# Kernel optimization log

Measured on AMD Instinct MI355X. Metric: run time of the kernel, lower is better.

## Reference

```python
import jax, jax.numpy as jnp
import numpy as np

N = 500_000      # evaluation points
M = 8            # Nmode
K = 4            # Clebsch branches
NPSI = 256       # psi grid points
X0 = 0.0
H = 1.0 / (NPSI - 1)


def _cubic_interp(f, x):
    """Cubic Hermite spline (C1, FD slopes) on a uniform psi grid, extrapolating.
    f: [NPSI, C] table, x: [N] query points -> [N, C]."""
    u = (x - X0) / H
    i = jnp.clip(jnp.floor(u).astype(jnp.int32), 0, NPSI - 2)
    s = (u - i.astype(x.dtype))[:, None]           # local coord, may be outside [0,1] (extrap)
    d = jnp.gradient(f, axis=0) / H                # FD derivatives [NPSI, C]
    f0, f1, d0, d1 = f[i], f[i + 1], d[i], d[i + 1]
    s2 = s * s
    s3 = s2 * s
    return ((2 * s3 - 3 * s2 + 1) * f0 + (s3 - 2 * s2 + s) * H * d0
            + (-2 * s3 + 3 * s2) * f1 + (s3 - s2) * H * d1)


def setup_inputs() -> dict:
    key = jax.random.key(0)
    ks = jax.random.split(key, 12)
    pg = jnp.linspace(0.0, 1.0, NPSI, dtype=jnp.float32)
    inp = {
        "t": jnp.float32(0.5),
        "psi": jax.random.uniform(ks[0], (N,), jnp.float32, 0.05, 0.95),
        "theta": jax.random.uniform(ks[1], (N,), jnp.float32, -jnp.pi, jnp.pi),
        "varphi": jax.random.uniform(ks[2], (N,), jnp.float32, 0.0, 2 * jnp.pi),
        # smooth Clebsch profiles on the psi grid (safety factor q and alpha offset)
        "q_vals": (1.0 + 2.5 * pg ** 2).astype(jnp.float32),
        "aoff_vals": (0.3 * jnp.sin(2 * jnp.pi * pg)).astype(jnp.float32),
        "theta0": jax.random.uniform(ks[3], (M,), jnp.float32, -jnp.pi, jnp.pi),
        "omega": jax.random.uniform(ks[4], (M,), jnp.float32, 0.5, 2.0),
        "psi0": jax.random.uniform(ks[5], (M,), jnp.float32, 0.2, 0.8),
        "psi_scale": jax.random.uniform(ks[6], (M,), jnp.float32, 0.05, 0.15),
        "alpha_scale": jax.random.uniform(ks[7], (M,), jnp.float32, 0.2, 0.6),
        "gh_coefs": 0.5 * jax.random.normal(ks[8], (M, 4, 6), jnp.float32),
        "n": jax.random.randint(ks[9], (M,), 1, 12, jnp.int32),
    }
    return inp


def reference(t, psi, theta, varphi, q_vals, aoff_vals, theta0, omega, psi0,
              psi_scale, alpha_scale, gh_coefs, n):
    # Clebsch mapping: alpha_k(psi, theta) = q(psi) * (theta + 2*pi*k) + alpha_off(psi)
    qa = _cubic_interp(jnp.stack([q_vals, aoff_vals], axis=-1), psi)  # [N,2]
    q, aoff = qa[:, 0], qa[:, 1]
    kk = 2 * jnp.pi * jnp.arange(K, dtype=psi.dtype)
    alpha = q[:, None] * (theta[:, None] + kk[None, :]) + aoff[:, None]    # [N,K]
    # alpha0(psi; mode) table built from the Clebsch profiles (mirrors __init__)
    alpha0_grid = q_vals[:, None] * theta0[None, :] + aoff_vals[:, None]   # [NPSI,M]
    alpha0 = _cubic_interp(alpha0_grid, psi)                               # [N,M]

    x = (psi[:, None] - psi0) / psi_scale                                  # [N,M]
    y = (alpha[:, None, :] - alpha0[:, :, None]) / alpha_scale[None, :, None]  # [N,M,K]
    g = jnp.exp(-0.5 * (x[:, :, None] ** 2 + y ** 2))                      # [N,M,K]

    c = gh_coefs  # [M,4,6]
    h10 = x[:, :, None, None]
    h01 = y[:, :, :, None]
    h20 = (4 * x ** 2 - 2)[:, :, None, None]
    h11 = (x[:, :, None] * y)[:, :, :, None]
    h02 = (4 * y ** 2 - 2)[:, :, :, None]
    p = (c[None, :, None, :, 0] + c[None, :, None, :, 1] * h10
         + c[None, :, None, :, 2] * h01 + c[None, :, None, :, 3] * h20
         + c[None, :, None, :, 4] * h11 + c[None, :, None, :, 5] * h02)    # [N,M,K,4]
    p = p * g[:, :, :, None]

    nf = n.astype(psi.dtype)
    # alpha - alpha0 == y * alpha_scale
    phase = omega[None, :, None] * t - nf[None, :, None] * (
        varphi[:, None, None] - y * alpha_scale[None, :, None])            # [N,M,K]
    cp, sp = jnp.cos(phase), jnp.sin(phase)
    phi = jnp.sum(p[..., 0] * cp - p[..., 1] * sp, axis=(1, 2))            # [N]
    apar = jnp.sum(p[..., 2] * cp - p[..., 3] * sp, axis=(1, 2))           # [N]
    return phi, apar
```

## Files before the change

kernel.cpp:

```cpp
#include <hip/hip_runtime.h>

#define NPSI 256
#define MM 8
#define KK 4

typedef float v2f __attribute__((ext_vector_type(2)));

#if __has_builtin(__builtin_amdgcn_exp2f)
#define EXP2F(x) __builtin_amdgcn_exp2f(x)
#else
#define EXP2F(x) exp2f(x)
#endif
#define SIN_REV(x) __builtin_amdgcn_sinf(x)
#define COS_REV(x) __builtin_amdgcn_cosf(x)

#define VFMA(a,b,c) __builtin_elementwise_fma((v2f)(a),(v2f)(b),(v2f)(c))

__device__ inline float cubic_q(const float* __restrict__ q_vals, float psi) {
    float u = psi * (float)(NPSI - 1);
    int   i = (int)floorf(u);
    i = min(max(i, 0), NPSI - 2);
    float s  = u - (float)i;
    float f0 = q_vals[i];
    float f1 = q_vals[i + 1];
    float d0 = (i == 0)        ? (f1 - f0) : 0.5f * (f1 - q_vals[i - 1]);
    float d1 = (i == NPSI - 2) ? (f1 - f0) : 0.5f * (q_vals[i + 2] - f0);
    float s2 = s * s, s3 = s2 * s;
    return (2.f * s3 - 3.f * s2 + 1.f) * f0
         + (s3 - 2.f * s2 + s)         * d0
         + (-2.f * s3 + 3.f * s2)      * f1
         + (s3 - s2)                   * d1;
}

__global__ __launch_bounds__(256, 8) void eik_kernel(
    const float* __restrict__ t_ptr,
    const float* __restrict__ psi_a,
    const float* __restrict__ theta_a,
    const float* __restrict__ varphi_a,
    const float* __restrict__ q_vals,
    const float* __restrict__ theta0_a,
    const float* __restrict__ omega_a,
    const float* __restrict__ psi0_a,
    const float* __restrict__ psi_scale_a,
    const float* __restrict__ alpha_scale_a,
    const float* __restrict__ gh_a,
    const int*   __restrict__ n_a,
    float* __restrict__ out,
    int N)
{
    const int gid = blockIdx.x * blockDim.x + threadIdx.x;
    if (gid >= N) return;

    const float INV2PI = 0.15915494309189533577f;
    const float TWO_PI = 6.28318530717958647692f;
    const float NEXPC  = -0.72134752044448170368f;

    const float t     = t_ptr[0];
    const float psi   = psi_a[gid];
    const float theta = theta_a[gid];
    const float vp    = varphi_a[gid] * INV2PI;

    const float q    = cubic_q(q_vals, psi);
    const float q2pi = q * TWO_PI;
    const float tt   = t * INV2PI;

    v2f phi = (v2f)0.f, apar = (v2f)0.f;

    #pragma unroll 1
    for (int mp = 0; mp < MM / 2; ++mp) {
        const int m = 2 * mp;
        const v2f theta0 = *(const v2f*)(theta0_a + m);
        const v2f omega  = *(const v2f*)(omega_a + m);
        const v2f psi0   = *(const v2f*)(psi0_a + m);
        const v2f psc    = *(const v2f*)(psi_scale_a + m);
        const v2f asc    = *(const v2f*)(alpha_scale_a + m);
        v2f inv_ps, inv_as, nf;
        inv_ps.x = __builtin_amdgcn_rcpf(psc.x);
        inv_ps.y = __builtin_amdgcn_rcpf(psc.y);
        inv_as.x = __builtin_amdgcn_rcpf(asc.x);
        inv_as.y = __builtin_amdgcn_rcpf(asc.y);
        nf.x = (float)n_a[m];
        nf.y = (float)n_a[m + 1];
        const float* cA = gh_a + m * 24;
        const float* cB = gh_a + (m + 1) * 24;

        const v2f x  = ((v2f)psi - psi0) * inv_ps;
        const v2f x2 = x * x;
        const v2f x4 = 4.f * x2;

        v2f pa[4], pb[4], pf[4];
        #pragma unroll
        for (int comp = 0; comp < 4; ++comp) {
            const v2f c0 = { cA[comp*6+0], cB[comp*6+0] };
            const v2f c1 = { cA[comp*6+1], cB[comp*6+1] };
            const v2f c2 = { cA[comp*6+2], cB[comp*6+2] };
            const v2f c3 = { cA[comp*6+3], cB[comp*6+3] };
            const v2f c4 = { cA[comp*6+4], cB[comp*6+4] };
            const v2f c5 = { cA[comp*6+5], cB[comp*6+5] };
            const v2f a0 = VFMA((v2f)(-2.f), c3 + c5, c0);
            pa[comp] = VFMA(c3, x4, VFMA(c1, x, a0));
            pb[comp] = VFMA(c4, x, c2);
            pf[comp] = c5;
        }

        const v2f dth  = (v2f)theta - theta0;
        const v2f qdth = q * dth;
        v2f y          = qdth * inv_as;
        const v2f dy   = q2pi * inv_as;
        const v2f dphr = nf * q;
        const v2f p0r  = VFMA(nf, qdth * INV2PI,
                              VFMA(omega, (v2f)tt, -nf * vp));

        v2f cp, sp, cd, sd;
        cp.x = COS_REV(p0r.x);  cp.y = COS_REV(p0r.y);
        sp.x = SIN_REV(p0r.x);  sp.y = SIN_REV(p0r.y);
        cd.x = COS_REV(dphr.x); cd.y = COS_REV(dphr.y);
        sd.x = SIN_REV(dphr.x); sd.y = SIN_REV(dphr.y);

        #pragma unroll
        for (int k = 0; k < KK; ++k) {
            const v2f t2 = VFMA(y, y, x2);
            const v2f y4 = VFMA((v2f)4.f, t2, -x4);
            const v2f ta = t2 * NEXPC;
            v2f g;
            g.x = EXP2F(ta.x);
            g.y = EXP2F(ta.y);
            const v2f gc = g * cp;
            const v2f gs = g * sp;
            const v2f p0 = VFMA(pf[0], y4, VFMA(pb[0], y, pa[0]));
            const v2f p1 = VFMA(pf[1], y4, VFMA(pb[1], y, pa[1]));
            const v2f p2 = VFMA(pf[2], y4, VFMA(pb[2], y, pa[2]));
            const v2f p3 = VFMA(pf[3], y4, VFMA(pb[3], y, pa[3]));
            phi  = VFMA(p0, gc, phi);
            phi  = VFMA(-p1, gs, phi);
            apar = VFMA(p2, gc, apar);
            apar = VFMA(-p3, gs, apar);
            if (k < KK - 1) {
                const v2f ncp = VFMA(cp, cd, -(sp * sd));
                const v2f nsp = VFMA(sp, cd,  cp * sd);
                cp = ncp; sp = nsp;
                y = y + dy;
            }
        }
    }

    out[gid]     = phi.x + phi.y;
    out[N + gid] = apar.x + apar.y;
}

extern "C" void kernel_launch(void* const* d_in, const int* in_sizes, int n_in,
                              void* d_out, int out_size, void* d_ws, size_t ws_size,
                              hipStream_t stream) {
    const float* t       = (const float*)d_in[0];
    const float* psi     = (const float*)d_in[1];
    const float* theta   = (const float*)d_in[2];
    const float* varphi  = (const float*)d_in[3];
    const float* q_vals  = (const float*)d_in[4];
    const float* theta0  = (const float*)d_in[6];
    const float* omega   = (const float*)d_in[7];
    const float* psi0    = (const float*)d_in[8];
    const float* psc     = (const float*)d_in[9];
    const float* asc     = (const float*)d_in[10];
    const float* gh      = (const float*)d_in[11];
    const int*   n_arr   = (const int*)d_in[12];

    const int N = in_sizes[1];
    float* out = (float*)d_out;

    const int block = 256;
    const int grid  = (N + block - 1) / block;
    eik_kernel<<<grid, block, 0, stream>>>(t, psi, theta, varphi, q_vals,
                                           theta0, omega, psi0, psc, asc,
                                           gh, n_arr, out, N);
}
```

Before: 97.26 us.

## Precompute per-mode constants in a prep kernel and batch exp evaluations

Adds a tiny prep kernel that writes per-mode constants (reciprocals of the scales, the folded polynomial coefficient, n as float) into a packed, interleaved workspace table. The main kernel then reads them as v2f pairs instead of gathering scalars and recomputing reciprocals and coefficient sums in every thread. The exp2 calls for all K branches are also hoisted into a separate loop ahead of the accumulation, to expose more independent transcendental work. The occupancy hint drops from 8 to 4 waves, which allows more registers per thread. The cost is an extra kernel launch and a workspace dependency.

```diff
diff --git a/kernel.cpp b/kernel.cpp
--- a/kernel.cpp
+++ b/kernel.cpp
@@ -3,6 +3,8 @@
 #define NPSI 256
 #define MM 8
 #define KK 4
+#define NMP (MM / 2)
+#define TBF (NMP * 60)
 
 typedef float v2f __attribute__((ext_vector_type(2)));
 
@@ -32,12 +34,7 @@
          + (s3 - s2)                   * d1;
 }
 
-__global__ __launch_bounds__(256, 8) void eik_kernel(
-    const float* __restrict__ t_ptr,
-    const float* __restrict__ psi_a,
-    const float* __restrict__ theta_a,
-    const float* __restrict__ varphi_a,
-    const float* __restrict__ q_vals,
+__global__ __launch_bounds__(64) void prep_kernel(
     const float* __restrict__ theta0_a,
     const float* __restrict__ omega_a,
     const float* __restrict__ psi0_a,
@@ -45,6 +42,41 @@
     const float* __restrict__ alpha_scale_a,
     const float* __restrict__ gh_a,
     const int*   __restrict__ n_a,
+    float* __restrict__ tb)
+{
+    const int tid = threadIdx.x;
+    if (tid < MM) {
+        const int m = tid, mp = m >> 1, lane = m & 1;
+        float* b = tb + mp * 60 + lane;
+        const float invps = 1.0f / psi_scale_a[m];
+        b[0]  = psi0_a[m] * invps;
+        b[2]  = invps;
+        b[4]  = 1.0f / alpha_scale_a[m];
+        b[6]  = (float)n_a[m];
+        b[8]  = theta0_a[m];
+        b[10] = omega_a[m];
+    }
+    if (tid < MM * 4) {
+        const int m = tid >> 2, comp = tid & 3;
+        const int mp = m >> 1, lane = m & 1;
+        const float* c = gh_a + m * 24 + comp * 6;
+        float* b = tb + mp * 60 + (6 + comp * 6) * 2 + lane;
+        b[0]  = fmaf(-2.f, c[3] + c[5], c[0]);
+        b[2]  = c[1];
+        b[4]  = c[3];
+        b[6]  = c[2];
+        b[8]  = c[4];
+        b[10] = c[5];
+    }
+}
+
+__global__ __launch_bounds__(256, 4) void eik_kernel(
+    const float* __restrict__ t_ptr,
+    const float* __restrict__ psi_a,
+    const float* __restrict__ theta_a,
+    const float* __restrict__ varphi_a,
+    const float* __restrict__ q_vals,
+    const float* __restrict__ tb,
     float* __restrict__ out,
     int N)
 {
@@ -67,49 +99,31 @@
     v2f phi = (v2f)0.f, apar = (v2f)0.f;
 
     #pragma unroll 1
-    for (int mp = 0; mp < MM / 2; ++mp) {
-        const int m = 2 * mp;
-        const v2f theta0 = *(const v2f*)(theta0_a + m);
-        const v2f omega  = *(const v2f*)(omega_a + m);
-        const v2f psi0   = *(const v2f*)(psi0_a + m);
-        const v2f psc    = *(const v2f*)(psi_scale_a + m);
-        const v2f asc    = *(const v2f*)(alpha_scale_a + m);
-        v2f inv_ps, inv_as, nf;
-        inv_ps.x = __builtin_amdgcn_rcpf(psc.x);
-        inv_ps.y = __builtin_amdgcn_rcpf(psc.y);
-        inv_as.x = __builtin_amdgcn_rcpf(asc.x);
-        inv_as.y = __builtin_amdgcn_rcpf(asc.y);
-        nf.x = (float)n_a[m];
-        nf.y = (float)n_a[m + 1];
-        const float* cA = gh_a + m * 24;
-        const float* cB = gh_a + (m + 1) * 24;
-
-        const v2f x  = ((v2f)psi - psi0) * inv_ps;
+    for (int mp = 0; mp < NMP; ++mp) {
+        const v2f* T = (const v2f*)tb + mp * 30;
+        const v2f psi0ps = T[0], invps = T[1], invas = T[2];
+        const v2f nf = T[3], th0 = T[4], om = T[5];
+
+        const v2f x  = VFMA((v2f)psi, invps, -psi0ps);
         const v2f x2 = x * x;
         const v2f x4 = 4.f * x2;
 
         v2f pa[4], pb[4], pf[4];
         #pragma unroll
         for (int comp = 0; comp < 4; ++comp) {
-            const v2f c0 = { cA[comp*6+0], cB[comp*6+0] };
-            const v2f c1 = { cA[comp*6+1], cB[comp*6+1] };
-            const v2f c2 = { cA[comp*6+2], cB[comp*6+2] };
-            const v2f c3 = { cA[comp*6+3], cB[comp*6+3] };
-            const v2f c4 = { cA[comp*6+4], cB[comp*6+4] };
-            const v2f c5 = { cA[comp*6+5], cB[comp*6+5] };
-            const v2f a0 = VFMA((v2f)(-2.f), c3 + c5, c0);
-            pa[comp] = VFMA(c3, x4, VFMA(c1, x, a0));
-            pb[comp] = VFMA(c4, x, c2);
-            pf[comp] = c5;
+            const v2f* B = T + 6 + comp * 6;
+            pa[comp] = VFMA(B[2], x4, VFMA(B[1], x, B[0]));
+            pb[comp] = VFMA(B[4], x, B[3]);
+            pf[comp] = B[5];
         }
 
-        const v2f dth  = (v2f)theta - theta0;
+        const v2f dth  = (v2f)theta - th0;
         const v2f qdth = q * dth;
-        v2f y          = qdth * inv_as;
-        const v2f dy   = q2pi * inv_as;
+        const v2f y0   = qdth * invas;
+        const v2f dy   = q2pi * invas;
         const v2f dphr = nf * q;
         const v2f p0r  = VFMA(nf, qdth * INV2PI,
-                              VFMA(omega, (v2f)tt, -nf * vp));
+                              VFMA(om, (v2f)tt, -nf * vp));
 
         v2f cp, sp, cd, sd;
         cp.x = COS_REV(p0r.x);  cp.y = COS_REV(p0r.y);
@@ -117,16 +131,26 @@
         cd.x = COS_REV(dphr.x); cd.y = COS_REV(dphr.y);
         sd.x = SIN_REV(dphr.x); sd.y = SIN_REV(dphr.y);
 
+        v2f t2v[KK], gv[KK];
+        {
+            v2f yk = y0;
+            #pragma unroll
+            for (int k = 0; k < KK; ++k) {
+                const v2f t2 = VFMA(yk, yk, x2);
+                t2v[k] = t2;
+                const v2f ta = t2 * NEXPC;
+                gv[k].x = EXP2F(ta.x);
+                gv[k].y = EXP2F(ta.y);
+                yk = yk + dy;
+            }
+        }
+
+        v2f y = y0;
         #pragma unroll
         for (int k = 0; k < KK; ++k) {
-            const v2f t2 = VFMA(y, y, x2);
-            const v2f y4 = VFMA((v2f)4.f, t2, -x4);
-            const v2f ta = t2 * NEXPC;
-            v2f g;
-            g.x = EXP2F(ta.x);
-            g.y = EXP2F(ta.y);
-            const v2f gc = g * cp;
-            const v2f gs = g * sp;
+            const v2f y4 = VFMA((v2f)4.f, t2v[k], -x4);
+            const v2f gc = gv[k] * cp;
+            const v2f gs = gv[k] * sp;
             const v2f p0 = VFMA(pf[0], y4, VFMA(pb[0], y, pa[0]));
             const v2f p1 = VFMA(pf[1], y4, VFMA(pb[1], y, pa[1]));
             const v2f p2 = VFMA(pf[2], y4, VFMA(pb[2], y, pa[2]));
@@ -166,10 +190,13 @@
 
     const int N = in_sizes[1];
     float* out = (float*)d_out;
+    float* tb  = (float*)d_ws;
+
+    prep_kernel<<<1, 64, 0, stream>>>(theta0, omega, psi0, psc, asc,
+                                      gh, n_arr, tb);
 
     const int block = 256;
     const int grid  = (N + block - 1) / block;
     eik_kernel<<<grid, block, 0, stream>>>(t, psi, theta, varphi, q_vals,
-                                           theta0, omega, psi0, psc, asc,
-                                           gh, n_arr, out, N);
-}
+                                           tb, out, N);
+}
```

Measured after the change: 93.02 us, median of 2. 4.4% less time.
